# Optimization experiments

Hardware: AMD Instinct MI355X
Metric: run time of the kernel (lower is better)

Reference implementation:

```python
import jax, jax.numpy as jnp
import numpy as np

N_NODES = 20000
N_EDGES = 320000
F_IN = 256
N_HID = 128
MID = 800


def _glorot(key, shape):
    fan_in, fan_out = shape
    s = jnp.sqrt(6.0 / (fan_in + fan_out))
    return jax.random.uniform(key, shape, jnp.float32, -s, s)


def setup_inputs() -> dict:
    key = jax.random.key(0)
    ks = jax.random.split(key, 8)
    x = jax.random.normal(ks[0], (N_NODES, F_IN), jnp.float32)
    src = jax.random.randint(ks[1], (N_EDGES,), 0, N_NODES)
    dst = jax.random.randint(ks[2], (N_EDGES,), 0, N_NODES)
    return {
        "x": x, "src": src, "dst": dst,
        "W1": _glorot(ks[3], (F_IN, MID)), "b1": jnp.zeros((MID,), jnp.float32),
        "W2": _glorot(ks[4], (MID, N_HID)), "b2": jnp.zeros((N_HID,), jnp.float32),
        "W3": _glorot(ks[5], (N_HID, MID)), "b3": jnp.zeros((MID,), jnp.float32),
        "W4": _glorot(ks[6], (MID, F_IN)), "b4": jnp.zeros((F_IN,), jnp.float32),
    }


def _deg_rsqrt(idx, n):
    # clamp(min=1) as in DGL GraphConv norm='both'
    deg = jax.ops.segment_sum(jnp.ones(idx.shape[0], jnp.float32), idx, num_segments=n)
    return jax.lax.rsqrt(jnp.maximum(deg, 1.0))


def _graph_conv(x, W, b, src, dst, n, act):
    # DGL GraphConv, norm='both': out = D_in^{-1/2} A D_out^{-1/2} X W + b
    ns = _deg_rsqrt(src, n)  # src-side (out-degree) norm
    nd = _deg_rsqrt(dst, n)  # dst-side (in-degree) norm
    in_f, out_f = W.shape
    if in_f > out_f:
        # multiply by W first (smaller aggregation width), as DGL does
        h = (x @ W) * ns[:, None]
        h = jax.ops.segment_sum(h[src], dst, num_segments=n)
    else:
        h = x * ns[:, None]
        h = jax.ops.segment_sum(h[src], dst, num_segments=n) @ W
    h = h * nd[:, None] + b
    return act(h) if act is not None else h


def reference(x, src, dst, W1, b1, W2, b2, W3, b3, W4, b4):
    n = x.shape[0]
    h = _graph_conv(x, W1, b1, src, dst, n, jax.nn.relu)   # [N, 800]
    h = _graph_conv(h, W2, b2, src, dst, n, None)          # [N, 128]
    encoded = jax.nn.sigmoid(h)
    h = _graph_conv(h, W3, b3, src, dst, n, jax.nn.relu)   # [N, 800]
    h = _graph_conv(h, W4, b4, src, dst, n, None)          # [N, 256]
    decoded = jax.nn.sigmoid(h)
    return (encoded, decoded)
```

## Files before the change

### kernel.cpp

```cpp
#include <hip/hip_runtime.h>
#include <math.h>

constexpr int NN = 20000;
constexpr int NE = 320000;
constexpr int MROWS = 20224;
constexpr int MH = 20096;
constexpr int SB = 79;

typedef __bf16 bf16x8 __attribute__((ext_vector_type(8)));
typedef float f32x4 __attribute__((ext_vector_type(4)));

__device__ __forceinline__ unsigned short f2bf(float f) {
  unsigned int u = __float_as_uint(f);
  unsigned int r = (u + 0x7FFFu + ((u >> 16) & 1u)) >> 16;
  return (unsigned short)r;
}

__device__ __forceinline__ int xcd_swizzle(int bid, int T) {
  int q = T >> 3, r = T & 7;
  int x = bid & 7, i = bid >> 3;
  return (x < r ? x * (q + 1) : r * (q + 1) + (x - r) * q) + i;
}

__global__ __launch_bounds__(256) void zero_kernel(int4* __restrict__ p, int n4) {
  int i = blockIdx.x * 256 + threadIdx.x;
  if (i < n4) p[i] = make_int4(0, 0, 0, 0);
}

__global__ void deg_count_kernel(const int* __restrict__ src, const int* __restrict__ dst,
                                 int* __restrict__ degs, int* __restrict__ degd, int nE) {
  int e = blockIdx.x * blockDim.x + threadIdx.x;
  if (e < nE) {
    atomicAdd(degs + src[e], 1);
    atomicAdd(degd + dst[e], 1);
  }
}

__global__ __launch_bounds__(256) void pscan_norm_kernel(
    const int* __restrict__ degs, const int* __restrict__ degd,
    int* __restrict__ pscan, int* __restrict__ bsum,
    float* __restrict__ ns, float* __restrict__ nd, int n) {
  __shared__ int s[256];
  int t = threadIdx.x;
  int idx = blockIdx.x * 256 + t;
  int val = 0;
  if (idx < n) {
    int dd = degd[idx];
    val = dd;
    ns[idx] = rsqrtf(fmaxf((float)degs[idx], 1.0f));
    nd[idx] = rsqrtf(fmaxf((float)dd, 1.0f));
  }
  s[t] = val;
  __syncthreads();
#pragma unroll
  for (int off = 1; off < 256; off <<= 1) {
    int v = (t >= off) ? s[t - off] : 0;
    __syncthreads();
    s[t] += v;
    __syncthreads();
  }
  if (idx < n) pscan[idx] = s[t] - val;
  if (t == 255) bsum[blockIdx.x] = s[255];
}

__global__ __launch_bounds__(128) void scan_off_kernel(
    const int* __restrict__ bsum, int* __restrict__ boff, int nb) {
  __shared__ int s[128];
  int t = threadIdx.x;
  int val = (t < nb) ? bsum[t] : 0;
  s[t] = val;
  __syncthreads();
#pragma unroll
  for (int off = 1; off < 128; off <<= 1) {
    int v = (t >= off) ? s[t - off] : 0;
    __syncthreads();
    s[t] += v;
    __syncthreads();
  }
  if (t < nb) boff[t] = s[t] - val;
}

__global__ __launch_bounds__(256) void rowptr_fix_kernel(
    const int* __restrict__ pscan, const int* __restrict__ boff,
    int* __restrict__ rowptr, int n) {
  int idx = blockIdx.x * 256 + threadIdx.x;
  if (idx < n) rowptr[idx] = pscan[idx] + boff[blockIdx.x];
  if (idx == 0) rowptr[n] = NE;
}

__global__ void csr_fill_kernel(const int* __restrict__ src, const int* __restrict__ dst,
                                const int* __restrict__ rowptr, int* __restrict__ cursor,
                                int* __restrict__ col, int nE) {
  int e = blockIdx.x * blockDim.x + threadIdx.x;
  if (e < nE) {
    int d = dst[e];
    int p = atomicAdd(cursor + d, 1);
    col[rowptr[d] + p] = src[e];
  }
}

__global__ __launch_bounds__(256) void wt_convert_all_kernel(
    const float* __restrict__ W1, const float* __restrict__ W2,
    const float* __restrict__ W3, const float* __restrict__ W4,
    unsigned short* __restrict__ W1t, unsigned short* __restrict__ W2t,
    unsigned short* __restrict__ W3t, unsigned short* __restrict__ W4t) {
  int n = blockIdx.y;
  int k = blockIdx.x * 256 + threadIdx.x;
  const float* W; unsigned short* Wt; int K, N, Kpad;
  if (n < 832)       { W = W1; Wt = W1t; K = 256; N = 800; Kpad = 256; }
  else if (n < 960)  { n -= 832;  W = W2; Wt = W2t; K = 800; N = 128; Kpad = 832; }
  else if (n < 1792) { n -= 960;  W = W3; Wt = W3t; K = 128; N = 800; Kpad = 128; }
  else               { n -= 1792; W = W4; Wt = W4t; K = 800; N = 256; Kpad = 832; }
  if (k >= Kpad) return;
  float v = (n < N && k < K) ? W[(size_t)k * N + n] : 0.f;
  Wt[(size_t)n * Kpad + k] = f2bf(v);
}

__global__ __launch_bounds__(256) void scale_cvt_kernel(
    const float* __restrict__ x, const float* __restrict__ ns,
    unsigned short* __restrict__ xb) {
  int t = blockIdx.x * 256 + threadIdx.x;
  if (t >= NN * 32) return;
  int node = t >> 5;
  float sc = ns[node];
  float4 v1 = reinterpret_cast<const float4*>(x)[t * 2];
  float4 v2 = reinterpret_cast<const float4*>(x)[t * 2 + 1];
  uint4 o;
  o.x = f2bf(v1.x * sc) | ((unsigned)f2bf(v1.y * sc) << 16);
  o.y = f2bf(v1.z * sc) | ((unsigned)f2bf(v1.w * sc) << 16);
  o.z = f2bf(v2.x * sc) | ((unsigned)f2bf(v2.y * sc) << 16);
  o.w = f2bf(v2.z * sc) | ((unsigned)f2bf(v2.w * sc) << 16);
  reinterpret_cast<uint4*>(xb)[t] = o;
}

template <int F, int EPI>
__global__ __launch_bounds__(256) void gatherb_kernel(
    const unsigned short* __restrict__ in, const int* __restrict__ rowptr,
    const int* __restrict__ col, const float* __restrict__ sDst,
    const float* __restrict__ bias, const float* __restrict__ snext,
    unsigned short* __restrict__ out, float* __restrict__ out2, int n) {
  constexpr int LPN = F / 8;
  constexpr int NPB = 256 / LPN;
  const int tid = threadIdx.x;
  const int node = blockIdx.x * NPB + tid / LPN;
  const int j = tid % LPN;
  if (node >= n) return;
  const int e0 = rowptr[node], e1 = rowptr[node + 1];
  float a[8] = {0.f, 0.f, 0.f, 0.f, 0.f, 0.f, 0.f, 0.f};
  int e = e0;
  for (; e + 1 < e1; e += 2) {
    int c0 = col[e], c1 = col[e + 1];
    uint4 u0 = *reinterpret_cast<const uint4*>(in + (size_t)c0 * F + j * 8);
    uint4 u1 = *reinterpret_cast<const uint4*>(in + (size_t)c1 * F + j * 8);
    a[0] += __uint_as_float(u0.x << 16);
    a[1] += __uint_as_float(u0.x & 0xffff0000u);
    a[2] += __uint_as_float(u0.y << 16);
    a[3] += __uint_as_float(u0.y & 0xffff0000u);
    a[4] += __uint_as_float(u0.z << 16);
    a[5] += __uint_as_float(u0.z & 0xffff0000u);
    a[6] += __uint_as_float(u0.w << 16);
    a[7] += __uint_as_float(u0.w & 0xffff0000u);
    a[0] += __uint_as_float(u1.x << 16);
    a[1] += __uint_as_float(u1.x & 0xffff0000u);
    a[2] += __uint_as_float(u1.y << 16);
    a[3] += __uint_as_float(u1.y & 0xffff0000u);
    a[4] += __uint_as_float(u1.z << 16);
    a[5] += __uint_as_float(u1.z & 0xffff0000u);
    a[6] += __uint_as_float(u1.w << 16);
    a[7] += __uint_as_float(u1.w & 0xffff0000u);
  }
  if (e < e1) {
    int c = col[e];
    uint4 u = *reinterpret_cast<const uint4*>(in + (size_t)c * F + j * 8);
    a[0] += __uint_as_float(u.x << 16);
    a[1] += __uint_as_float(u.x & 0xffff0000u);
    a[2] += __uint_as_float(u.y << 16);
    a[3] += __uint_as_float(u.y & 0xffff0000u);
    a[4] += __uint_as_float(u.z << 16);
    a[5] += __uint_as_float(u.z & 0xffff0000u);
    a[6] += __uint_as_float(u.w << 16);
    a[7] += __uint_as_float(u.w & 0xffff0000u);
  }
  if (EPI == 0) {
    uint4 o;
    o.x = f2bf(a[0]) | ((unsigned)f2bf(a[1]) << 16);
    o.y = f2bf(a[2]) | ((unsigned)f2bf(a[3]) << 16);
    o.z = f2bf(a[4]) | ((unsigned)f2bf(a[5]) << 16);
    o.w = f2bf(a[6]) | ((unsigned)f2bf(a[7]) << 16);
    *reinterpret_cast<uint4*>(out + (size_t)node * F + j * 8) = o;
    return;
  }
  const float sd = sDst[node];
  float v[8];
#pragma unroll
  for (int k = 0; k < 8; ++k) v[k] = a[k] * sd + bias[j * 8 + k];
  if (EPI == 1) {
    float sn = snext[node];
    uint4 o;
    o.x = f2bf(v[0] * sn) | ((unsigned)f2bf(v[1] * sn) << 16);
    o.y = f2bf(v[2] * sn) | ((unsigned)f2bf(v[3] * sn) << 16);
    o.z = f2bf(v[4] * sn) | ((unsigned)f2bf(v[5] * sn) << 16);
    o.w = f2bf(v[6] * sn) | ((unsigned)f2bf(v[7] * sn) << 16);
    *reinterpret_cast<uint4*>(out + (size_t)node * F + j * 8) = o;
  }
  float4 s1, s2;
  s1.x = 1.0f / (1.0f + expf(-v[0]));
  s1.y = 1.0f / (1.0f + expf(-v[1]));
  s1.z = 1.0f / (1.0f + expf(-v[2]));
  s1.w = 1.0f / (1.0f + expf(-v[3]));
  s2.x = 1.0f / (1.0f + expf(-v[4]));
  s2.y = 1.0f / (1.0f + expf(-v[5]));
  s2.z = 1.0f / (1.0f + expf(-v[6]));
  s2.w = 1.0f / (1.0f + expf(-v[7]));
  *reinterpret_cast<float4*>(out2 + (size_t)node * F + j * 8) = s1;
  *reinterpret_cast<float4*>(out2 + (size_t)node * F + j * 8 + 4) = s2;
}

template <int KT, int RELU>
__global__ __launch_bounds__(256) void gemm8s_kernel(
    const unsigned short* __restrict__ A, const unsigned short* __restrict__ Bt,
    unsigned short* __restrict__ C, int M, int Nreal, int NTn,
    const float* __restrict__ rowscale, const float* __restrict__ bias) {
  constexpr int K = KT * 32;
  constexpr int CPR = KT * 4;
  constexpr int ROWB = CPR * 16;
  constexpr int TC = 64 * CPR;
  __shared__ __align__(16) char lds[64 * ROWB];

  const int sw = xcd_swizzle(blockIdx.x, gridDim.x);
  const int mg = sw / NTn, nt = sw - mg * NTn;
  const int tid = threadIdx.x;
  const int l = tid & 63, w = tid >> 6;
  const int lrow = l & 15, k16 = l >> 4;
  const int m0 = mg * 128 + w * 32, n0 = nt * 64;

#pragma unroll
  for (int i = 0; i < TC / 256; ++i) {
    int c = i * 256 + tid;
    int row = c / CPR, lch = c % CPR;
    int gch = (lch & ~7) | ((lch & 7) ^ (row & 7));
    const unsigned short* gp = Bt + (size_t)(n0 + row) * K + gch * 8;
    __builtin_amdgcn_global_load_lds(
        (const __attribute__((address_space(1))) void*)gp,
        (__attribute__((address_space(3))) void*)(lds + (i * 256 + w * 64) * 16), 16, 0, 0);
  }

  bf16x8 af[KT][2];
#pragma unroll
  for (int t = 0; t < KT; ++t)
#pragma unroll
    for (int mi = 0; mi < 2; ++mi)
      af[t][mi] = *reinterpret_cast<const bf16x8*>(
          A + (size_t)(m0 + mi * 16 + lrow) * K + t * 32 + k16 * 8);

  __syncthreads();

  f32x4 acc[2][4] = {};
#pragma unroll
  for (int t = 0; t < KT; ++t) {
    bf16x8 bf[4];
#pragma unroll
    for (int ni = 0; ni < 4; ++ni) {
      int row = ni * 16 + lrow;
      int ch = t * 4 + k16;
      int sc = (ch & ~7) | ((ch & 7) ^ (row & 7));
      bf[ni] = *reinterpret_cast<const bf16x8*>(lds + row * ROWB + sc * 16);
    }
#pragma unroll
    for (int mi = 0; mi < 2; ++mi)
#pragma unroll
      for (int ni = 0; ni < 4; ++ni)
        acc[mi][ni] = __builtin_amdgcn_mfma_f32_16x16x32_bf16(af[t][mi], bf[ni], acc[mi][ni], 0, 0, 0);
  }

#pragma unroll
  for (int mi = 0; mi < 2; ++mi) {
#pragma unroll
    for (int q = 0; q < 4; ++q) {
      int r = m0 + mi * 16 + k16 * 4 + q;
      if (r >= M) continue;
      float rs = rowscale[r];
#pragma unroll
      for (int ni = 0; ni < 4; ++ni) {
        int c = n0 + ni * 16 + lrow;
        if (c >= Nreal) continue;
        float v = acc[mi][ni][q] * rs + bias[c];
        if (RELU) v = fmaxf(v, 0.f);
        C[(size_t)r * Nreal + c] = f2bf(v);
      }
    }
  }
}

template <int OUT_BF>
__global__ __launch_bounds__(256) void gemm8l_kernel(
    const unsigned short* __restrict__ A, const unsigned short* __restrict__ Bt,
    void* __restrict__ C, int M, int N, int NTn,
    const float* __restrict__ rowscale) {
  constexpr int K = 800, KPAD = 832;
  constexpr int CPR = 52;
  constexpr int ROWB = CPR * 16;
  __shared__ __align__(16) char lds[64 * ROWB];

  const int sw = xcd_swizzle(blockIdx.x, gridDim.x);
  const int mg = sw / NTn, nt = sw - mg * NTn;
  const int tid = threadIdx.x;
  const int l = tid & 63, w = tid >> 6;
  const int lrow = l & 15, k16 = l >> 4;
  const int m0 = mg * 128 + w * 32, n0 = nt * 64;

  auto stage = [&](int phase) {
#pragma unroll
    for (int i = 0; i < 13; ++i) {
      int c = i * 256 + tid;
      int row = c / CPR, lch = c % CPR;
      int gch = phase * CPR + ((lch & ~3) | ((lch & 3) ^ (row & 3)));
      const unsigned short* gp = Bt + (size_t)(n0 + row) * KPAD + gch * 8;
      __builtin_amdgcn_global_load_lds(
          (const __attribute__((address_space(1))) void*)gp,
          (__attribute__((address_space(3))) void*)(lds + (i * 256 + w * 64) * 16), 16, 0, 0);
    }
  };

  f32x4 acc[2][4] = {};

  auto compute = [&](int t0, int t1, int phase) {
#pragma unroll 13
    for (int t = t0; t < t1; ++t) {
      bf16x8 a[2];
#pragma unroll
      for (int mi = 0; mi < 2; ++mi)
        a[mi] = *reinterpret_cast<const bf16x8*>(
            A + (size_t)(m0 + mi * 16 + lrow) * K + t * 32 + k16 * 8);
      bf16x8 bf[4];
#pragma unroll
      for (int ni = 0; ni < 4; ++ni) {
        int row = ni * 16 + lrow;
        int ch = t * 4 + k16 - phase * CPR;
        int sc = (ch & ~3) | ((ch & 3) ^ (row & 3));
        bf[ni] = *reinterpret_cast<const bf16x8*>(lds + row * ROWB + sc * 16);
      }
#pragma unroll
      for (int mi = 0; mi < 2; ++mi)
#pragma unroll
        for (int ni = 0; ni < 4; ++ni)
          acc[mi][ni] = __builtin_amdgcn_mfma_f32_16x16x32_bf16(a[mi], bf[ni], acc[mi][ni], 0, 0, 0);
    }
  };

  stage(0);
  __syncthreads();
  compute(0, 13, 0);
  __syncthreads();
  stage(1);
  __syncthreads();
  compute(13, 25, 1);

#pragma unroll
  for (int mi = 0; mi < 2; ++mi) {
#pragma unroll
    for (int q = 0; q < 4; ++q) {
      int r = m0 + mi * 16 + k16 * 4 + q;
      if (r >= M) continue;
      float rs = rowscale[r];
#pragma unroll
      for (int ni = 0; ni < 4; ++ni) {
        int c = n0 + ni * 16 + lrow;
        float v = acc[mi][ni][q] * rs;
        if (OUT_BF) ((unsigned short*)C)[(size_t)r * N + c] = f2bf(v);
        else ((float*)C)[(size_t)r * N + c] = v;
      }
    }
  }
}

extern "C" void kernel_launch(void* const* d_in, const int* in_sizes, int n_in,
                              void* d_out, int out_size, void* d_ws, size_t ws_size,
                              hipStream_t stream) {
  const float* x  = (const float*)d_in[0];
  const int* src  = (const int*)d_in[1];
  const int* dst  = (const int*)d_in[2];
  const float* W1 = (const float*)d_in[3];
  const float* b1 = (const float*)d_in[4];
  const float* W2 = (const float*)d_in[5];
  const float* b2 = (const float*)d_in[6];
  const float* W3 = (const float*)d_in[7];
  const float* b3 = (const float*)d_in[8];
  const float* W4 = (const float*)d_in[9];
  const float* b4 = (const float*)d_in[10];

  float* out_enc = (float*)d_out;
  float* out_dec = out_enc + (size_t)NN * 128;

  float* ns = (float*)d_ws;
  float* nd = ns + NN;
  unsigned short* xb  = (unsigned short*)(nd + NN);
  unsigned short* T2b = xb + (size_t)NN * 256;
  unsigned short* h2  = T2b + (size_t)NN * 128;
  unsigned short* A1  = h2 + (size_t)NN * 128;
  unsigned short* A3  = A1 + (size_t)MROWS * 256;
  unsigned short* G4  = A3 + (size_t)MROWS * 128;
  unsigned short* H1  = G4 + (size_t)NN * 256;
  unsigned short* W1t = H1 + (size_t)MH * 800;
  unsigned short* W2t = W1t + 832 * 256;
  unsigned short* W3t = W2t + 128 * 832;
  unsigned short* W4t = W3t + 832 * 128;
  int* degs   = (int*)(W4t + 256 * 832);
  int* degd   = degs + NN;
  int* cursor = degd + NN;
  int* rowptr = cursor + NN;
  int* col    = rowptr + NN + 1;
  int* pscan  = col + NE;
  int* bsum   = pscan + NN;
  int* boff   = bsum + SB;

  zero_kernel<<<(3 * NN / 4 + 255) / 256, 256, 0, stream>>>((int4*)degs, 3 * NN / 4);
  deg_count_kernel<<<(NE + 255) / 256, 256, 0, stream>>>(src, dst, degs, degd, NE);
  pscan_norm_kernel<<<SB, 256, 0, stream>>>(degs, degd, pscan, bsum, ns, nd, NN);
  scan_off_kernel<<<1, 128, 0, stream>>>(bsum, boff, SB);
  rowptr_fix_kernel<<<SB, 256, 0, stream>>>(pscan, boff, rowptr, NN);
  csr_fill_kernel<<<(NE + 255) / 256, 256, 0, stream>>>(src, dst, rowptr, cursor, col, NE);

  wt_convert_all_kernel<<<dim3(4, 2048), 256, 0, stream>>>(
      W1, W2, W3, W4, W1t, W2t, W3t, W4t);

  const int GS = 157 * 13;
  const int GL2 = 157 * 2;
  const int GL4 = 157 * 4;

  scale_cvt_kernel<<<(NN * 32 + 255) / 256, 256, 0, stream>>>(x, ns, xb);
  gatherb_kernel<256, 0><<<(NN + 7) / 8, 256, 0, stream>>>(
      xb, rowptr, col, nullptr, nullptr, nullptr, A1, nullptr, NN);
  gemm8s_kernel<8, 1><<<GS, 256, 0, stream>>>(A1, W1t, H1, NN, 800, 13, nd, b1);

  gemm8l_kernel<1><<<GL2, 256, 0, stream>>>(H1, W2t, T2b, NN, 128, 2, ns);
  gatherb_kernel<128, 1><<<(NN + 15) / 16, 256, 0, stream>>>(
      T2b, rowptr, col, nd, b2, ns, h2, out_enc, NN);

  gatherb_kernel<128, 0><<<(NN + 15) / 16, 256, 0, stream>>>(
      h2, rowptr, col, nullptr, nullptr, nullptr, A3, nullptr, NN);
  gemm8s_kernel<4, 1><<<GS, 256, 0, stream>>>(A3, W3t, H1, NN, 800, 13, nd, b3);

  gemm8l_kernel<1><<<GL4, 256, 0, stream>>>(H1, W4t, G4, NN, 256, 4, ns);
  gatherb_kernel<256, 2><<<(NN + 7) / 8, 256, 0, stream>>>(
      G4, rowptr, col, nd, b4, nullptr, nullptr, out_dec, NN);
}
```

Before: 253.1 us.

## Fuse layer-1 and layer-2 GEMMs, keeping the hidden tile in LDS; merge scan kernels

New measurement: 247.3 us. 2.3% less time.

```diff
diff --git a/kernel.cpp b/kernel.cpp
--- a/kernel.cpp
+++ b/kernel.cpp
@@ -63,28 +63,23 @@
   if (t == 255) bsum[blockIdx.x] = s[255];
 }
 
-__global__ __launch_bounds__(128) void scan_off_kernel(
-    const int* __restrict__ bsum, int* __restrict__ boff, int nb) {
+__global__ __launch_bounds__(256) void rowptr_fix_kernel(
+    const int* __restrict__ pscan, const int* __restrict__ bsum,
+    int* __restrict__ rowptr, int n) {
   __shared__ int s[128];
   int t = threadIdx.x;
-  int val = (t < nb) ? bsum[t] : 0;
-  s[t] = val;
+  if (t < 128) s[t] = (t < SB) ? bsum[t] : 0;
   __syncthreads();
 #pragma unroll
   for (int off = 1; off < 128; off <<= 1) {
-    int v = (t >= off) ? s[t - off] : 0;
+    int v = (t < 128 && t >= off) ? s[t - off] : 0;
     __syncthreads();
-    s[t] += v;
+    if (t < 128) s[t] += v;
     __syncthreads();
   }
-  if (t < nb) boff[t] = s[t] - val;
-}
-
-__global__ __launch_bounds__(256) void rowptr_fix_kernel(
-    const int* __restrict__ pscan, const int* __restrict__ boff,
-    int* __restrict__ rowptr, int n) {
-  int idx = blockIdx.x * 256 + threadIdx.x;
-  if (idx < n) rowptr[idx] = pscan[idx] + boff[blockIdx.x];
+  int idx = blockIdx.x * 256 + t;
+  int boff = (blockIdx.x == 0) ? 0 : s[blockIdx.x - 1];
+  if (idx < n) rowptr[idx] = pscan[idx] + boff;
   if (idx == 0) rowptr[n] = NE;
 }
 
@@ -216,6 +211,137 @@
   *reinterpret_cast<float4*>(out2 + (size_t)node * F + j * 8 + 4) = s2;
 }
 
+__global__ __launch_bounds__(256) void gemm9f_kernel(
+    const unsigned short* __restrict__ A,
+    const unsigned short* __restrict__ W1t,
+    const unsigned short* __restrict__ W2t,
+    unsigned short* __restrict__ T2b,
+    int M, const float* __restrict__ nd, const float* __restrict__ ns,
+    const float* __restrict__ b1) {
+  __shared__ __align__(16) char lds[112 * 1024];
+  const int tid = threadIdx.x;
+  const int l = tid & 63, w = tid >> 6;
+  const int lrow = l & 15, k16 = l >> 4;
+  const int m0 = blockIdx.x * 128 + w * 32;
+  char* const h1t = lds + 98304 + w * 4096;
+
+  auto stage = [&](int buf, int nt) {
+    char* w1p = lds + buf * 32768;
+    char* w2s = lds + 65536 + buf * 16384;
+#pragma unroll
+    for (int i = 0; i < 8; ++i) {
+      int c = i * 256 + tid;
+      int row = c >> 5, lch = c & 31;
+      int gch = (lch & ~7) | ((lch & 7) ^ (row & 7));
+      const unsigned short* gp = W1t + (size_t)(nt * 64 + row) * 256 + gch * 8;
+      __builtin_amdgcn_global_load_lds(
+          (const __attribute__((address_space(1))) void*)gp,
+          (__attribute__((address_space(3))) void*)(w1p + (i * 256 + w * 64) * 16), 16, 0, 0);
+    }
+#pragma unroll
+    for (int i = 0; i < 4; ++i) {
+      int c = i * 256 + tid;
+      int row = c >> 3, lch = c & 7;
+      int gch = lch ^ (row & 7);
+      const unsigned short* gp = W2t + (size_t)row * 832 + nt * 64 + gch * 8;
+      __builtin_amdgcn_global_load_lds(
+          (const __attribute__((address_space(1))) void*)gp,
+          (__attribute__((address_space(3))) void*)(w2s + (i * 256 + w * 64) * 16), 16, 0, 0);
+    }
+  };
+
+  bf16x8 af[8][2];
+#pragma unroll
+  for (int t = 0; t < 8; ++t)
+#pragma unroll
+    for (int mi = 0; mi < 2; ++mi)
+      af[t][mi] = *reinterpret_cast<const bf16x8*>(
+          A + (size_t)(m0 + mi * 16 + lrow) * 256 + t * 32 + k16 * 8);
+
+  stage(0, 0);
+  __syncthreads();
+
+  f32x4 acc2[2][8] = {};
+  for (int nt = 0; nt < 13; ++nt) {
+    const int cur = nt & 1;
+    if (nt + 1 < 13) stage(cur ^ 1, nt + 1);
+    const char* w1p = lds + cur * 32768;
+    const char* w2s = lds + 65536 + cur * 16384;
+
+    f32x4 acc1[2][4] = {};
+#pragma unroll
+    for (int t = 0; t < 8; ++t) {
+      bf16x8 bf[4];
+#pragma unroll
+      for (int ni = 0; ni < 4; ++ni) {
+        int row = ni * 16 + lrow;
+        int ch = t * 4 + k16;
+        int sc = (ch & ~7) | ((ch & 7) ^ (row & 7));
+        bf[ni] = *reinterpret_cast<const bf16x8*>(w1p + row * 512 + sc * 16);
+      }
+#pragma unroll
+      for (int mi = 0; mi < 2; ++mi)
+#pragma unroll
+        for (int ni = 0; ni < 4; ++ni)
+          acc1[mi][ni] = __builtin_amdgcn_mfma_f32_16x16x32_bf16(af[t][mi], bf[ni], acc1[mi][ni], 0, 0, 0);
+    }
+
+#pragma unroll
+    for (int mi = 0; mi < 2; ++mi) {
+#pragma unroll
+      for (int q = 0; q < 4; ++q) {
+        int rl = mi * 16 + k16 * 4 + q;
+        float rs = nd[m0 + rl];
+#pragma unroll
+        for (int ni = 0; ni < 4; ++ni) {
+          int colc = ni * 16 + lrow;
+          int jg = nt * 64 + colc;
+          float bb = (jg < 800) ? b1[jg] : 0.f;
+          float v = fmaxf(acc1[mi][ni][q] * rs + bb, 0.f);
+          int sc = (colc >> 3) ^ (rl & 7);
+          *(unsigned short*)(h1t + rl * 128 + sc * 16 + (colc & 7) * 2) = f2bf(v);
+        }
+      }
+    }
+
+#pragma unroll
+    for (int ks = 0; ks < 2; ++ks) {
+      bf16x8 a2[2];
+#pragma unroll
+      for (int mi = 0; mi < 2; ++mi) {
+        int rl = mi * 16 + lrow;
+        int sc = (ks * 4 + k16) ^ (rl & 7);
+        a2[mi] = *reinterpret_cast<const bf16x8*>(h1t + rl * 128 + sc * 16);
+      }
+#pragma unroll
+      for (int ni = 0; ni < 8; ++ni) {
+        int rc = ni * 16 + lrow;
+        int sc = (ks * 4 + k16) ^ (rc & 7);
+        bf16x8 b2v = *reinterpret_cast<const bf16x8*>(w2s + rc * 128 + sc * 16);
+#pragma unroll
+        for (int mi = 0; mi < 2; ++mi)
+          acc2[mi][ni] = __builtin_amdgcn_mfma_f32_16x16x32_bf16(a2[mi], b2v, acc2[mi][ni], 0, 0, 0);
+      }
+    }
+    __syncthreads();
+  }
+
+#pragma unroll
+  for (int mi = 0; mi < 2; ++mi) {
+#pragma unroll
+    for (int q = 0; q < 4; ++q) {
+      int r = m0 + mi * 16 + k16 * 4 + q;
+      if (r >= M) continue;
+      float sn = ns[r];
+#pragma unroll
+      for (int ni = 0; ni < 8; ++ni) {
+        int c = ni * 16 + lrow;
+        T2b[(size_t)r * 128 + c] = f2bf(acc2[mi][ni][q] * sn);
+      }
+    }
+  }
+}
+
 template <int KT, int RELU>
 __global__ __launch_bounds__(256) void gemm8s_kernel(
     const unsigned short* __restrict__ A, const unsigned short* __restrict__ Bt,
@@ -412,28 +538,24 @@
   int* col    = rowptr + NN + 1;
   int* pscan  = col + NE;
   int* bsum   = pscan + NN;
-  int* boff   = bsum + SB;
 
   zero_kernel<<<(3 * NN / 4 + 255) / 256, 256, 0, stream>>>((int4*)degs, 3 * NN / 4);
   deg_count_kernel<<<(NE + 255) / 256, 256, 0, stream>>>(src, dst, degs, degd, NE);
   pscan_norm_kernel<<<SB, 256, 0, stream>>>(degs, degd, pscan, bsum, ns, nd, NN);
-  scan_off_kernel<<<1, 128, 0, stream>>>(bsum, boff, SB);
-  rowptr_fix_kernel<<<SB, 256, 0, stream>>>(pscan, boff, rowptr, NN);
+  rowptr_fix_kernel<<<SB, 256, 0, stream>>>(pscan, bsum, rowptr, NN);
   csr_fill_kernel<<<(NE + 255) / 256, 256, 0, stream>>>(src, dst, rowptr, cursor, col, NE);
 
   wt_convert_all_kernel<<<dim3(4, 2048), 256, 0, stream>>>(
       W1, W2, W3, W4, W1t, W2t, W3t, W4t);
 
   const int GS = 157 * 13;
-  const int GL2 = 157 * 2;
   const int GL4 = 157 * 4;
 
   scale_cvt_kernel<<<(NN * 32 + 255) / 256, 256, 0, stream>>>(x, ns, xb);
   gatherb_kernel<256, 0><<<(NN + 7) / 8, 256, 0, stream>>>(
       xb, rowptr, col, nullptr, nullptr, nullptr, A1, nullptr, NN);
-  gemm8s_kernel<8, 1><<<GS, 256, 0, stream>>>(A1, W1t, H1, NN, 800, 13, nd, b1);
-
-  gemm8l_kernel<1><<<GL2, 256, 0, stream>>>(H1, W2t, T2b, NN, 128, 2, ns);
+  gemm9f_kernel<<<157, 256, 0, stream>>>(A1, W1t, W2t, T2b, NN, nd, ns, b1);
+
   gatherb_kernel<128, 1><<<(NN + 15) / 16, 256, 0, stream>>>(
       T2b, rowptr, col, nd, b2, ns, h2, out_enc, NN);
 
```

## Fuse back-to-back GEMMs through the 800-wide hidden layer and merge scan kernels

Applied to the files above, without the earlier changes.

Measured after the change: 245.0 us. 3.2% less time.

```diff
diff --git a/kernel.cpp b/kernel.cpp
--- a/kernel.cpp
+++ b/kernel.cpp
@@ -4,7 +4,6 @@
 constexpr int NN = 20000;
 constexpr int NE = 320000;
 constexpr int MROWS = 20224;
-constexpr int MH = 20096;
 constexpr int SB = 79;
 
 typedef __bf16 bf16x8 __attribute__((ext_vector_type(8)));
@@ -14,12 +13,6 @@
   unsigned int u = __float_as_uint(f);
   unsigned int r = (u + 0x7FFFu + ((u >> 16) & 1u)) >> 16;
   return (unsigned short)r;
-}
-
-__device__ __forceinline__ int xcd_swizzle(int bid, int T) {
-  int q = T >> 3, r = T & 7;
-  int x = bid & 7, i = bid >> 3;
-  return (x < r ? x * (q + 1) : r * (q + 1) + (x - r) * q) + i;
 }
 
 __global__ __launch_bounds__(256) void zero_kernel(int4* __restrict__ p, int n4) {
@@ -63,28 +56,23 @@
   if (t == 255) bsum[blockIdx.x] = s[255];
 }
 
-__global__ __launch_bounds__(128) void scan_off_kernel(
-    const int* __restrict__ bsum, int* __restrict__ boff, int nb) {
+__global__ __launch_bounds__(256) void rowptr_fix_kernel(
+    const int* __restrict__ pscan, const int* __restrict__ bsum,
+    int* __restrict__ rowptr, int n) {
   __shared__ int s[128];
   int t = threadIdx.x;
-  int val = (t < nb) ? bsum[t] : 0;
-  s[t] = val;
+  if (t < 128) s[t] = (t < SB) ? bsum[t] : 0;
   __syncthreads();
 #pragma unroll
   for (int off = 1; off < 128; off <<= 1) {
-    int v = (t >= off) ? s[t - off] : 0;
-    __syncthreads();
-    s[t] += v;
-    __syncthreads();
-  }
-  if (t < nb) boff[t] = s[t] - val;
-}
-
-__global__ __launch_bounds__(256) void rowptr_fix_kernel(
-    const int* __restrict__ pscan, const int* __restrict__ boff,
-    int* __restrict__ rowptr, int n) {
-  int idx = blockIdx.x * 256 + threadIdx.x;
-  if (idx < n) rowptr[idx] = pscan[idx] + boff[blockIdx.x];
+    int v = (t < 128 && t >= off) ? s[t - off] : 0;
+    __syncthreads();
+    if (t < 128) s[t] += v;
+    __syncthreads();
+  }
+  int idx = blockIdx.x * 256 + t;
+  int boff = (blockIdx.x == 0) ? 0 : s[blockIdx.x - 1];
+  if (idx < n) rowptr[idx] = pscan[idx] + boff;
   if (idx == 0) rowptr[n] = NE;
 }
 
@@ -216,160 +204,122 @@
   *reinterpret_cast<float4*>(out2 + (size_t)node * F + j * 8 + 4) = s2;
 }
 
-template <int KT, int RELU>
-__global__ __launch_bounds__(256) void gemm8s_kernel(
-    const unsigned short* __restrict__ A, const unsigned short* __restrict__ Bt,
-    unsigned short* __restrict__ C, int M, int Nreal, int NTn,
-    const float* __restrict__ rowscale, const float* __restrict__ bias) {
-  constexpr int K = KT * 32;
-  constexpr int CPR = KT * 4;
-  constexpr int ROWB = CPR * 16;
-  constexpr int TC = 64 * CPR;
-  __shared__ __align__(16) char lds[64 * ROWB];
-
-  const int sw = xcd_swizzle(blockIdx.x, gridDim.x);
-  const int mg = sw / NTn, nt = sw - mg * NTn;
+template <int KT1, int NOUT>
+__global__ __launch_bounds__(256) void gemm9v2_kernel(
+    const unsigned short* __restrict__ A,
+    const unsigned short* __restrict__ Wa,
+    const unsigned short* __restrict__ Wb,
+    unsigned short* __restrict__ Out,
+    int M, const float* __restrict__ nd, const float* __restrict__ ns,
+    const float* __restrict__ ba) {
+  constexpr int K1 = KT1 * 32;
+  constexpr int N2 = NOUT * 16;
+  constexpr int ROWB1 = K1 * 2;
+  constexpr int CPR1 = K1 / 8;
+  constexpr int W1B = 64 * ROWB1;
+  constexpr int W2B = N2 * 128;
+  constexpr int HST = 144;
+  __shared__ __align__(16) char lds[W1B + W2B + 4 * 16 * HST];
+
   const int tid = threadIdx.x;
   const int l = tid & 63, w = tid >> 6;
   const int lrow = l & 15, k16 = l >> 4;
-  const int m0 = mg * 128 + w * 32, n0 = nt * 64;
-
-#pragma unroll
-  for (int i = 0; i < TC / 256; ++i) {
-    int c = i * 256 + tid;
-    int row = c / CPR, lch = c % CPR;
-    int gch = (lch & ~7) | ((lch & 7) ^ (row & 7));
-    const unsigned short* gp = Bt + (size_t)(n0 + row) * K + gch * 8;
-    __builtin_amdgcn_global_load_lds(
-        (const __attribute__((address_space(1))) void*)gp,
-        (__attribute__((address_space(3))) void*)(lds + (i * 256 + w * 64) * 16), 16, 0, 0);
-  }
-
-  bf16x8 af[KT][2];
-#pragma unroll
-  for (int t = 0; t < KT; ++t)
-#pragma unroll
-    for (int mi = 0; mi < 2; ++mi)
-      af[t][mi] = *reinterpret_cast<const bf16x8*>(
-          A + (size_t)(m0 + mi * 16 + lrow) * K + t * 32 + k16 * 8);
-
-  __syncthreads();
-
-  f32x4 acc[2][4] = {};
-#pragma unroll
-  for (int t = 0; t < KT; ++t) {
-    bf16x8 bf[4];
-#pragma unroll
-    for (int ni = 0; ni < 4; ++ni) {
-      int row = ni * 16 + lrow;
-      int ch = t * 4 + k16;
-      int sc = (ch & ~7) | ((ch & 7) ^ (row & 7));
-      bf[ni] = *reinterpret_cast<const bf16x8*>(lds + row * ROWB + sc * 16);
-    }
-#pragma unroll
-    for (int mi = 0; mi < 2; ++mi)
-#pragma unroll
-      for (int ni = 0; ni < 4; ++ni)
-        acc[mi][ni] = __builtin_amdgcn_mfma_f32_16x16x32_bf16(af[t][mi], bf[ni], acc[mi][ni], 0, 0, 0);
-  }
-
-#pragma unroll
-  for (int mi = 0; mi < 2; ++mi) {
-#pragma unroll
-    for (int q = 0; q < 4; ++q) {
-      int r = m0 + mi * 16 + k16 * 4 + q;
-      if (r >= M) continue;
-      float rs = rowscale[r];
-#pragma unroll
-      for (int ni = 0; ni < 4; ++ni) {
-        int c = n0 + ni * 16 + lrow;
-        if (c >= Nreal) continue;
-        float v = acc[mi][ni][q] * rs + bias[c];
-        if (RELU) v = fmaxf(v, 0.f);
-        C[(size_t)r * Nreal + c] = f2bf(v);
-      }
-    }
-  }
-}
-
-template <int OUT_BF>
-__global__ __launch_bounds__(256) void gemm8l_kernel(
-    const unsigned short* __restrict__ A, const unsigned short* __restrict__ Bt,
-    void* __restrict__ C, int M, int N, int NTn,
-    const float* __restrict__ rowscale) {
-  constexpr int K = 800, KPAD = 832;
-  constexpr int CPR = 52;
-  constexpr int ROWB = CPR * 16;
-  __shared__ __align__(16) char lds[64 * ROWB];
-
-  const int sw = xcd_swizzle(blockIdx.x, gridDim.x);
-  const int mg = sw / NTn, nt = sw - mg * NTn;
-  const int tid = threadIdx.x;
-  const int l = tid & 63, w = tid >> 6;
-  const int lrow = l & 15, k16 = l >> 4;
-  const int m0 = mg * 128 + w * 32, n0 = nt * 64;
-
-  auto stage = [&](int phase) {
-#pragma unroll
-    for (int i = 0; i < 13; ++i) {
+  const int m0 = blockIdx.x * 64 + w * 16;
+  char* const w1p = lds;
+  char* const w2s = lds + W1B;
+  char* const h1t = lds + W1B + W2B + w * 16 * HST;
+
+  auto stage = [&](int nt) {
+#pragma unroll
+    for (int i = 0; i < 64 * CPR1 / 256; ++i) {
       int c = i * 256 + tid;
-      int row = c / CPR, lch = c % CPR;
-      int gch = phase * CPR + ((lch & ~3) | ((lch & 3) ^ (row & 3)));
-      const unsigned short* gp = Bt + (size_t)(n0 + row) * KPAD + gch * 8;
+      int row = c / CPR1, lch = c % CPR1;
+      int gch = (lch & ~7) | ((lch & 7) ^ (row & 7));
+      const unsigned short* gp = Wa + (size_t)(nt * 64 + row) * K1 + gch * 8;
       __builtin_amdgcn_global_load_lds(
           (const __attribute__((address_space(1))) void*)gp,
-          (__attribute__((address_space(3))) void*)(lds + (i * 256 + w * 64) * 16), 16, 0, 0);
+          (__attribute__((address_space(3))) void*)(w1p + (i * 256 + w * 64) * 16), 16, 0, 0);
+    }
+#pragma unroll
+    for (int i = 0; i < N2 * 8 / 256; ++i) {
+      int c = i * 256 + tid;
+      int row = c >> 3, lch = c & 7;
+      int gch = lch ^ (row & 7);
+      const unsigned short* gp = Wb + (size_t)row * 832 + nt * 64 + gch * 8;
+      __builtin_amdgcn_global_load_lds(
+          (const __attribute__((address_space(1))) void*)gp,
+          (__attribute__((address_space(3))) void*)(w2s + (i * 256 + w * 64) * 16), 16, 0, 0);
     }
   };
 
-  f32x4 acc[2][4] = {};
-
-  auto compute = [&](int t0, int t1, int phase) {
-#pragma unroll 13
-    for (int t = t0; t < t1; ++t) {
-      bf16x8 a[2];
-#pragma unroll
-      for (int mi = 0; mi < 2; ++mi)
-        a[mi] = *reinterpret_cast<const bf16x8*>(
-            A + (size_t)(m0 + mi * 16 + lrow) * K + t * 32 + k16 * 8);
+  bf16x8 af[KT1];
+#pragma unroll
+  for (int t = 0; t < KT1; ++t)
+    af[t] = *reinterpret_cast<const bf16x8*>(
+        A + (size_t)(m0 + lrow) * K1 + t * 32 + k16 * 8);
+
+  stage(0);
+  __syncthreads();
+
+  f32x4 acc2[NOUT] = {};
+  for (int nt = 0; nt < 13; ++nt) {
+    f32x4 acc1[4] = {};
+#pragma unroll
+    for (int t = 0; t < KT1; ++t) {
       bf16x8 bf[4];
 #pragma unroll
       for (int ni = 0; ni < 4; ++ni) {
         int row = ni * 16 + lrow;
-        int ch = t * 4 + k16 - phase * CPR;
-        int sc = (ch & ~3) | ((ch & 3) ^ (row & 3));
-        bf[ni] = *reinterpret_cast<const bf16x8*>(lds + row * ROWB + sc * 16);
+        int ch = t * 4 + k16;
+        int sc = (ch & ~7) | ((ch & 7) ^ (row & 7));
+        bf[ni] = *reinterpret_cast<const bf16x8*>(w1p + row * ROWB1 + sc * 16);
       }
 #pragma unroll
-      for (int mi = 0; mi < 2; ++mi)
-#pragma unroll
-        for (int ni = 0; ni < 4; ++ni)
-          acc[mi][ni] = __builtin_amdgcn_mfma_f32_16x16x32_bf16(a[mi], bf[ni], acc[mi][ni], 0, 0, 0);
-    }
-  };
-
-  stage(0);
-  __syncthreads();
-  compute(0, 13, 0);
-  __syncthreads();
-  stage(1);
-  __syncthreads();
-  compute(13, 25, 1);
-
-#pragma unroll
-  for (int mi = 0; mi < 2; ++mi) {
+      for (int ni = 0; ni < 4; ++ni)
+        acc1[ni] = __builtin_amdgcn_mfma_f32_16x16x32_bf16(af[t], bf[ni], acc1[ni], 0, 0, 0);
+    }
+
 #pragma unroll
     for (int q = 0; q < 4; ++q) {
-      int r = m0 + mi * 16 + k16 * 4 + q;
-      if (r >= M) continue;
-      float rs = rowscale[r];
+      int rl = k16 * 4 + q;
+      float rs = nd[m0 + rl];
 #pragma unroll
       for (int ni = 0; ni < 4; ++ni) {
-        int c = n0 + ni * 16 + lrow;
-        float v = acc[mi][ni][q] * rs;
-        if (OUT_BF) ((unsigned short*)C)[(size_t)r * N + c] = f2bf(v);
-        else ((float*)C)[(size_t)r * N + c] = v;
+        int colc = ni * 16 + lrow;
+        int jg = nt * 64 + colc;
+        float bb = (jg < 800) ? ba[jg] : 0.f;
+        float v = fmaxf(acc1[ni][q] * rs + bb, 0.f);
+        *(unsigned short*)(h1t + rl * HST + (colc >> 3) * 16 + (colc & 7) * 2) = f2bf(v);
       }
+    }
+
+#pragma unroll
+    for (int ks = 0; ks < 2; ++ks) {
+      bf16x8 a2 = *reinterpret_cast<const bf16x8*>(h1t + lrow * HST + (ks * 4 + k16) * 16);
+#pragma unroll
+      for (int ni = 0; ni < NOUT; ++ni) {
+        int rc = ni * 16 + lrow;
+        int sc = (ks * 4 + k16) ^ (rc & 7);
+        bf16x8 b2v = *reinterpret_cast<const bf16x8*>(w2s + rc * 128 + sc * 16);
+        acc2[ni] = __builtin_amdgcn_mfma_f32_16x16x32_bf16(a2, b2v, acc2[ni], 0, 0, 0);
+      }
+    }
+    __syncthreads();
+    if (nt + 1 < 13) {
+      stage(nt + 1);
+      __syncthreads();
+    }
+  }
+
+#pragma unroll
+  for (int q = 0; q < 4; ++q) {
+    int r = m0 + k16 * 4 + q;
+    if (r >= M) continue;
+    float sn = ns[r];
+#pragma unroll
+    for (int ni = 0; ni < NOUT; ++ni) {
+      int c = ni * 16 + lrow;
+      Out[(size_t)r * N2 + c] = f2bf(acc2[ni][q] * sn);
     }
   }
 }
@@ -400,8 +350,7 @@
   unsigned short* A1  = h2 + (size_t)NN * 128;
   unsigned short* A3  = A1 + (size_t)MROWS * 256;
   unsigned short* G4  = A3 + (size_t)MROWS * 128;
-  unsigned short* H1  = G4 + (size_t)NN * 256;
-  unsigned short* W1t = H1 + (size_t)MH * 800;
+  unsigned short* W1t = G4 + (size_t)NN * 256;
   unsigned short* W2t = W1t + 832 * 256;
   unsigned short* W3t = W2t + 128 * 832;
   unsigned short* W4t = W3t + 832 * 128;
@@ -412,36 +361,28 @@
   int* col    = rowptr + NN + 1;
   int* pscan  = col + NE;
   int* bsum   = pscan + NN;
-  int* boff   = bsum + SB;
 
   zero_kernel<<<(3 * NN / 4 + 255) / 256, 256, 0, stream>>>((int4*)degs, 3 * NN / 4);
   deg_count_kernel<<<(NE + 255) / 256, 256, 0, stream>>>(src, dst, degs, degd, NE);
   pscan_norm_kernel<<<SB, 256, 0, stream>>>(degs, degd, pscan, bsum, ns, nd, NN);
-  scan_off_kernel<<<1, 128, 0, stream>>>(bsum, boff, SB);
-  rowptr_fix_kernel<<<SB, 256, 0, stream>>>(pscan, boff, rowptr, NN);
+  rowptr_fix_kernel<<<SB, 256, 0, stream>>>(pscan, bsum, rowptr, NN);
   csr_fill_kernel<<<(NE + 255) / 256, 256, 0, stream>>>(src, dst, rowptr, cursor, col, NE);
 
   wt_convert_all_kernel<<<dim3(4, 2048), 256, 0, stream>>>(
       W1, W2, W3, W4, W1t, W2t, W3t, W4t);
-
-  const int GS = 157 * 13;
-  const int GL2 = 157 * 2;
-  const int GL4 = 157 * 4;
 
   scale_cvt_kernel<<<(NN * 32 + 255) / 256, 256, 0, stream>>>(x, ns, xb);
   gatherb_kernel<256, 0><<<(NN + 7) / 8, 256, 0, stream>>>(
       xb, rowptr, col, nullptr, nullptr, nullptr, A1, nullptr, NN);
-  gemm8s_kernel<8, 1><<<GS, 256, 0, stream>>>(A1, W1t, H1, NN, 800, 13, nd, b1);
-
-  gemm8l_kernel<1><<<GL2, 256, 0, stream>>>(H1, W2t, T2b, NN, 128, 2, ns);
+  gemm9v2_kernel<8, 8><<<314, 256, 0, stream>>>(A1, W1t, W2t, T2b, NN, nd, ns, b1);
+
   gatherb_kernel<128, 1><<<(NN + 15) / 16, 256, 0, stream>>>(
       T2b, rowptr, col, nd, b2, ns, h2, out_enc, NN);
 
   gatherb_kernel<128, 0><<<(NN + 15) / 16, 256, 0, stream>>>(
       h2, rowptr, col, nullptr, nullptr, nullptr, A3, nullptr, NN);
-  gemm8s_kernel<4, 1><<<GS, 256, 0, stream>>>(A3, W3t, H1, NN, 800, 13, nd, b3);
-
-  gemm8l_kernel<1><<<GL4, 256, 0, stream>>>(H1, W4t, G4, NN, 256, 4, ns);
+  gemm9v2_kernel<4, 16><<<314, 256, 0, stream>>>(A3, W3t, W4t, G4, NN, nd, ns, b3);
+
   gatherb_kernel<256, 2><<<(NN + 7) / 8, 256, 0, stream>>>(
       G4, rowptr, col, nd, b4, nullptr, nullptr, out_dec, NN);
 }
```
